# Kernel tuning notes

Hardware: AMD Instinct MI355X
Metric: run time of the kernel (lower is better)

Reference implementation:

```python
import jax, jax.numpy as jnp
import numpy as np

ALPHA = 0.025
BETA = 0.00025
V_TH = 1.0
EXP_TAU = 50.0          # tau_v / dt
T_NOW = 10.0            # current simulation step counter self.t
REFRAC_STEPS = 2        # refractory_period / dt
INV_TAU_V = float(np.exp(-1.0 / 50.0))   # exp(-dt/tau_v)
INV_TAU_I = float(np.exp(-1.0))          # exp(-dt/tau_i)
INV_TAU_V_PAIR = INV_TAU_V               # tau_v_pair defaults to tau_v
INV_TAU_I_PAIR = INV_TAU_I               # tau_i_pair defaults to tau_i

B, N = 32, 4096


def setup_inputs() -> dict:
    key = jax.random.key(0)
    ks = jax.random.split(key, 8)
    return {
        "inp": jax.random.normal(ks[0], (B, N), jnp.float32),
        "W_rec": jax.random.uniform(ks[1], (N, N), jnp.float32),  # nonneg dense adjacency weights
        "mem_pot": jax.random.normal(ks[2], (B, N), jnp.float32),
        "mem_cur": jax.random.normal(ks[3], (B, N), jnp.float32),
        "mem_pot_paired": jax.random.normal(ks[4], (B, N), jnp.float32),
        "mem_cur_paired": jax.random.normal(ks[5], (B, N), jnp.float32),
        "st": jnp.zeros((N,), jnp.float32),
        "refrac_neurons": jax.random.randint(ks[6], (B, N), 0, 3, jnp.int32),
    }


def reference(inp, W_rec, mem_pot, mem_cur, mem_pot_paired, mem_cur_paired, st, refrac_neurons):
    sign_mask = W_rec > 0  # torch: sign(W_rec) > 0 (weights are nonneg)

    # decrement refractory counters
    refrac = jnp.where(refrac_neurons > 0, refrac_neurons - 1, refrac_neurons)

    # threshold (ceil+clamp -> {0,1} spikes)
    S = jnp.clip(jnp.ceil(mem_pot - V_TH), 0.0, 1.0)                     # (B,N)
    S_paired = jnp.clip(jnp.ceil(mem_pot_paired - V_TH - ALPHA), 0.0, 1.0)

    # ---- plasticity weight update ----
    sp_max = S_paired.max(axis=0)            # (N,)
    st_new = jnp.where(S > 0, T_NOW, st)     # broadcasts (N,) -> (B,N), as in torch
    max_st = st_new.max(axis=0)              # (N,)
    # meshgrid(a,b) with ij indexing: |a-b|[i,j] = |max_st[i]-max_st[j]|
    diff = jnp.abs(max_st[:, None] - max_st[None, :])                    # (N,N)
    update_mask = (sp_max[:, None] > 0) & sign_mask                      # (N,N)
    updated = W_rec + BETA - jnp.where(update_mask,
                                       ALPHA * jnp.exp(diff / EXP_TAU),
                                       0.0)
    updated = jnp.clip(updated, 0.0, 1.0)
    W_new = jnp.where(sign_mask, updated, W_rec)

    # ---- integrate ----
    active = refrac == 0
    mem_cur_n = jnp.where(active, inp + S @ W_new + mem_cur, mem_cur)
    mem_cur_p_n = jnp.where(active, S @ W_new.T + mem_cur_paired, mem_cur_paired)
    mem_pot_n = jnp.where(active, mem_cur_n + mem_pot, mem_pot)
    mem_pot_p_n = jnp.where(active, mem_cur_p_n + mem_pot_paired, mem_pot_paired)

    # leak
    mem_pot_n = mem_pot_n * INV_TAU_V
    mem_cur_n = mem_cur_n * INV_TAU_I
    mem_pot_p_n = mem_pot_p_n * INV_TAU_V_PAIR
    mem_cur_p_n = mem_cur_p_n * INV_TAU_I_PAIR

    # reset spiked neurons
    mem_pot_n = jnp.where(S > 0, 0.0, mem_pot_n)
    mem_pot_p_n = jnp.where(S_paired > 0, 0.0, mem_pot_p_n)
    refrac_new = jnp.where(S > 0, REFRAC_STEPS, refrac)

    return S, mem_pot_n, W_new, mem_cur_n, mem_pot_p_n, mem_cur_p_n, refrac_new
```

## Files before the change

kernel.cpp:

```cpp
#include <hip/hip_runtime.h>
#include <cstdint>
#include <cstddef>

constexpr int N = 4096;
constexpr int B = 32;
constexpr int BN = B * N;
constexpr size_t NN = (size_t)N * N;
constexpr int KCHUNKS = 8;
constexpr int KC = N / KCHUNKS;

constexpr float ALPHA = 0.025f;
constexpr float BETA = 0.00025f;
constexpr float T_NOW = 10.0f;
constexpr float INV_EXP_TAU = 0.02f;
constexpr float INV_TAU_V = 0.98019867f;
constexpr float INV_TAU_I = 0.36787944f;

typedef __attribute__((ext_vector_type(8))) short short8;
typedef __attribute__((ext_vector_type(4))) float f32x4;

__device__ inline unsigned short f2bf(float f) {
  uint32_t u = __float_as_uint(f);
  u += 0x7FFFu + ((u >> 16) & 1u);
  return (unsigned short)(u >> 16);
}

__device__ inline float wupd(float w, float mrow, float frow, float mcol) {
  float d = fabsf(mrow - mcol);
  float u = w + BETA - frow * __expf(d * INV_EXP_TAU);
  u = fminf(fmaxf(u, 0.0f), 1.0f);
  return (w > 0.0f) ? u : w;
}

__global__ __launch_bounds__(256) void pass_a(
    const float* __restrict__ mem_pot, const float* __restrict__ mem_pot_p,
    const float* __restrict__ st, float* __restrict__ S_out,
    unsigned short* __restrict__ S_bf,
    uint32_t* __restrict__ maskS, uint32_t* __restrict__ maskSP,
    float* __restrict__ max_st, float* __restrict__ rowfac,
    float4* __restrict__ zero_region ) {
  int j = blockIdx.x * blockDim.x + threadIdx.x;
  if (j >= N) return;

  float4 z = {0.0f, 0.0f, 0.0f, 0.0f};
  #pragma unroll
  for (int k = 0; k < 16; ++k) zero_region[j + k * 4096] = z;

  float stj = st[j];
  uint32_t ms = 0u, msp = 0u;
  float maxv = -3.0e38f;
  #pragma unroll
  for (int b = 0; b < B; ++b) {
    float p = mem_pot[b * N + j];
    float pp = mem_pot_p[b * N + j];
    bool s = (p - 1.0f) > 0.0f;
    bool sp = ((pp - 1.0f) - ALPHA) > 0.0f;
    S_out[b * N + j] = s ? 1.0f : 0.0f;
    S_bf[b * N + j] = s ? 0x3F80u : 0u;
    ms |= (uint32_t)s << b;
    msp |= (uint32_t)sp << b;
    maxv = fmaxf(maxv, s ? T_NOW : stj);
  }
  maskS[j] = ms;
  maskSP[j] = msp;
  max_st[j] = maxv;
  rowfac[j] = msp ? ALPHA : 0.0f;
}

__global__ __launch_bounds__(256) void pass_fused(
    const float* __restrict__ W, const unsigned short* __restrict__ S_bf,
    const float* __restrict__ max_st, const float* __restrict__ rowfac,
    float* __restrict__ Wout, float* __restrict__ SW, float* __restrict__ SWT) {
  __shared__ float mstK[KC];
  __shared__ float facK[KC];

  int tid = threadIdx.x;
  int wv = tid >> 6;
  int lane = tid & 63;
  int ntile = blockIdx.x * 4 + wv;
  int j0 = ntile * 16;
  int kbase = blockIdx.y * KC;
  int gemm = blockIdx.z;
  int quad = lane >> 4;
  int nl = lane & 15;

  for (int t = tid; t < KC; t += 256) {
    mstK[t] = max_st[kbase + t];
    facK[t] = rowfac[kbase + t];
  }
  __syncthreads();

  f32x4 acc0 = {0.f, 0.f, 0.f, 0.f};
  f32x4 acc1 = {0.f, 0.f, 0.f, 0.f};
  const unsigned short* A0p = S_bf + (size_t)nl * N;
  const unsigned short* A1p = S_bf + (size_t)(nl + 16) * N;

  if (gemm == 0) {
    float mj = max_st[j0 + nl];
    #pragma unroll 2
    for (int it = 0; it < KC / 32; ++it) {
      int ko = it * 32 + quad * 8;
      int kg = kbase + ko;
      short8 a0 = *(const short8*)(A0p + kg);
      short8 a1 = *(const short8*)(A1p + kg);
      const float* wp = W + (size_t)kg * N + j0 + nl;
      float4 m4a = *(const float4*)(mstK + ko);
      float4 m4b = *(const float4*)(mstK + ko + 4);
      float4 f4a = *(const float4*)(facK + ko);
      float4 f4b = *(const float4*)(facK + ko + 4);
      float w[8];
      #pragma unroll
      for (int i = 0; i < 8; ++i) w[i] = wp[(size_t)i * N];
      short8 bf;
      bf[0] = (short)f2bf(wupd(w[0], m4a.x, f4a.x, mj));
      bf[1] = (short)f2bf(wupd(w[1], m4a.y, f4a.y, mj));
      bf[2] = (short)f2bf(wupd(w[2], m4a.z, f4a.z, mj));
      bf[3] = (short)f2bf(wupd(w[3], m4a.w, f4a.w, mj));
      bf[4] = (short)f2bf(wupd(w[4], m4b.x, f4b.x, mj));
      bf[5] = (short)f2bf(wupd(w[5], m4b.y, f4b.y, mj));
      bf[6] = (short)f2bf(wupd(w[6], m4b.z, f4b.z, mj));
      bf[7] = (short)f2bf(wupd(w[7], m4b.w, f4b.w, mj));
      acc0 = __builtin_amdgcn_mfma_f32_16x16x32_bf16(a0, bf, acc0, 0, 0, 0);
      acc1 = __builtin_amdgcn_mfma_f32_16x16x32_bf16(a1, bf, acc1, 0, 0, 0);
    }
  } else {
    float mi = max_st[j0 + nl];
    float fi = rowfac[j0 + nl];
    const float* __restrict__ Wr = W + (size_t)(j0 + nl) * N;
    float* __restrict__ Wor = Wout + (size_t)(j0 + nl) * N;
    #pragma unroll 2
    for (int it = 0; it < KC / 32; ++it) {
      int ko = it * 32 + quad * 8;
      int kg = kbase + ko;
      short8 a0 = *(const short8*)(A0p + kg);
      short8 a1 = *(const short8*)(A1p + kg);
      float4 f0 = *(const float4*)(Wr + kg);
      float4 f1 = *(const float4*)(Wr + kg + 4);
      float4 m4a = *(const float4*)(mstK + ko);
      float4 m4b = *(const float4*)(mstK + ko + 4);
      float4 u0, u1;
      u0.x = wupd(f0.x, mi, fi, m4a.x);
      u0.y = wupd(f0.y, mi, fi, m4a.y);
      u0.z = wupd(f0.z, mi, fi, m4a.z);
      u0.w = wupd(f0.w, mi, fi, m4a.w);
      u1.x = wupd(f1.x, mi, fi, m4b.x);
      u1.y = wupd(f1.y, mi, fi, m4b.y);
      u1.z = wupd(f1.z, mi, fi, m4b.z);
      u1.w = wupd(f1.w, mi, fi, m4b.w);
      *(float4*)(Wor + kg) = u0;
      *(float4*)(Wor + kg + 4) = u1;
      short8 bf;
      bf[0] = (short)f2bf(u0.x); bf[1] = (short)f2bf(u0.y);
      bf[2] = (short)f2bf(u0.z); bf[3] = (short)f2bf(u0.w);
      bf[4] = (short)f2bf(u1.x); bf[5] = (short)f2bf(u1.y);
      bf[6] = (short)f2bf(u1.z); bf[7] = (short)f2bf(u1.w);
      acc0 = __builtin_amdgcn_mfma_f32_16x16x32_bf16(a0, bf, acc0, 0, 0, 0);
      acc1 = __builtin_amdgcn_mfma_f32_16x16x32_bf16(a1, bf, acc1, 0, 0, 0);
    }
  }

  float* dst = (gemm == 0) ? SW : SWT;
  #pragma unroll
  for (int r = 0; r < 4; ++r) {
    atomicAdd(dst + (size_t)(quad * 4 + r) * N + j0 + nl, acc0[r]);
    atomicAdd(dst + (size_t)(16 + quad * 4 + r) * N + j0 + nl, acc1[r]);
  }
}

__global__ __launch_bounds__(256) void pass_d(
    const float* __restrict__ inp, const float* __restrict__ mem_pot,
    const float* __restrict__ mem_cur, const float* __restrict__ mem_pot_p,
    const float* __restrict__ mem_cur_p, const int* __restrict__ refrac_in,
    const uint32_t* __restrict__ maskS, const uint32_t* __restrict__ maskSP,
    const float* __restrict__ SWbuf, const float* __restrict__ SWTbuf,
    float* __restrict__ pot_out, float* __restrict__ cur_out,
    float* __restrict__ potp_out, float* __restrict__ curp_out,
    float* __restrict__ refrac_out) {
  int e = blockIdx.x * 256 + threadIdx.x;
  int b = e >> 12;
  int j = e & (N - 1);

  float SW = SWbuf[e];
  float SWT = SWTbuf[e];

  int r = refrac_in[e];
  int rd = (r > 0) ? (r - 1) : r;
  bool active = (rd == 0);
  bool s = (maskS[j] >> b) & 1u;
  bool sp = (maskSP[j] >> b) & 1u;
  float cur = mem_cur[e], pot = mem_pot[e];
  float curp = mem_cur_p[e], potp = mem_pot_p[e];

  float cur_n = active ? (inp[e] + SW + cur) : cur;
  float curp_n = active ? (SWT + curp) : curp;
  float pot_n = active ? (cur_n + pot) : pot;
  float potp_n = active ? (curp_n + potp) : potp;

  pot_n *= INV_TAU_V;
  cur_n *= INV_TAU_I;
  potp_n *= INV_TAU_V;
  curp_n *= INV_TAU_I;

  if (s) pot_n = 0.0f;
  if (sp) potp_n = 0.0f;
  int rn = s ? 2 : rd;

  pot_out[e] = pot_n;
  cur_out[e] = cur_n;
  potp_out[e] = potp_n;
  curp_out[e] = curp_n;
  refrac_out[e] = (float)rn;
}

extern "C" void kernel_launch(void* const* d_in, const int* in_sizes, int n_in,
                              void* d_out, int out_size, void* d_ws, size_t ws_size,
                              hipStream_t stream) {
  const float* inp = (const float*)d_in[0];
  const float* W = (const float*)d_in[1];
  const float* mem_pot = (const float*)d_in[2];
  const float* mem_cur = (const float*)d_in[3];
  const float* mem_pot_p = (const float*)d_in[4];
  const float* mem_cur_p = (const float*)d_in[5];
  const float* st = (const float*)d_in[6];
  const int* refrac = (const int*)d_in[7];

  float* out = (float*)d_out;
  float* S_out = out;
  float* pot_out = out + BN;
  float* W_out = out + 2 * (size_t)BN;
  float* cur_out = W_out + NN;
  float* potp_out = cur_out + BN;
  float* curp_out = potp_out + BN;
  float* refrac_out = curp_out + BN;

  uint32_t* maskS = (uint32_t*)d_ws;
  uint32_t* maskSP = maskS + N;
  float* max_st = (float*)(maskSP + N);
  float* rowfac = max_st + N;
  unsigned short* S_bf = (unsigned short*)(rowfac + N);
  float* SW = (float*)(S_bf + BN);
  float* SWT = SW + BN;

  pass_a<<<N / 256, 256, 0, stream>>>(mem_pot, mem_pot_p, st, S_out, S_bf,
                                      maskS, maskSP, max_st, rowfac,
                                      (float4*)SW);
  pass_fused<<<dim3(64, KCHUNKS, 2), 256, 0, stream>>>(W, S_bf, max_st, rowfac,
                                                       W_out, SW, SWT);
  pass_d<<<BN / 256, 256, 0, stream>>>(inp, mem_pot, mem_cur, mem_pot_p,
                                       mem_cur_p, refrac, maskS, maskSP,
                                       SW, SWT, pot_out, cur_out,
                                       potp_out, curp_out, refrac_out);
}
```

Before: 171.2 us.

## Replace atomic split-K accumulation with per-chunk partials and in-block LDS reduction

Each block now covers one 16-column tile, and its four waves split that block's K chunk among themselves. The per-wave MFMA accumulators are summed through shared memory, and each block writes a plain partial sum per K chunk. The final pass adds the four partials instead of relying on atomicAdd into zeroed buffers, so the zeroing in pass_a goes away. The W loads are software-prefetched one iteration ahead, and launch bounds request higher occupancy. In exchange the workspace traffic for partials grows, and the reduction adds a block-wide barrier.

New measurement: 175.8 us. +2.6%, slower.

```diff
diff --git a/kernel.cpp b/kernel.cpp
--- a/kernel.cpp
+++ b/kernel.cpp
@@ -6,8 +6,10 @@
 constexpr int B = 32;
 constexpr int BN = B * N;
 constexpr size_t NN = (size_t)N * N;
-constexpr int KCHUNKS = 8;
-constexpr int KC = N / KCHUNKS;
+constexpr int KCHUNKS = 4;
+constexpr int CHUNK = N / KCHUNKS;
+constexpr int KW = CHUNK / 4;
+constexpr int NIT = KW / 32;
 
 constexpr float ALPHA = 0.025f;
 constexpr float BETA = 0.00025f;
@@ -37,15 +39,9 @@
     const float* __restrict__ st, float* __restrict__ S_out,
     unsigned short* __restrict__ S_bf,
     uint32_t* __restrict__ maskS, uint32_t* __restrict__ maskSP,
-    float* __restrict__ max_st, float* __restrict__ rowfac,
-    float4* __restrict__ zero_region ) {
+    float* __restrict__ max_st, float* __restrict__ rowfac) {
   int j = blockIdx.x * blockDim.x + threadIdx.x;
   if (j >= N) return;
-
-  float4 z = {0.0f, 0.0f, 0.0f, 0.0f};
-  #pragma unroll
-  for (int k = 0; k < 16; ++k) zero_region[j + k * 4096] = z;
-
   float stj = st[j];
   uint32_t ms = 0u, msp = 0u;
   float maxv = -3.0e38f;
@@ -67,24 +63,25 @@
   rowfac[j] = msp ? ALPHA : 0.0f;
 }
 
-__global__ __launch_bounds__(256) void pass_fused(
+__global__ __launch_bounds__(256, 6) void pass_fused(
     const float* __restrict__ W, const unsigned short* __restrict__ S_bf,
     const float* __restrict__ max_st, const float* __restrict__ rowfac,
-    float* __restrict__ Wout, float* __restrict__ SW, float* __restrict__ SWT) {
-  __shared__ float mstK[KC];
-  __shared__ float facK[KC];
+    float* __restrict__ Wout, float* __restrict__ partSW,
+    float* __restrict__ partSWT) {
+  __shared__ float mstK[CHUNK];
+  __shared__ float facK[CHUNK];
+  __shared__ float red[4][32][17];
 
   int tid = threadIdx.x;
   int wv = tid >> 6;
   int lane = tid & 63;
-  int ntile = blockIdx.x * 4 + wv;
-  int j0 = ntile * 16;
-  int kbase = blockIdx.y * KC;
+  int j0 = blockIdx.x * 16;
+  int kbase = blockIdx.y * CHUNK;
   int gemm = blockIdx.z;
   int quad = lane >> 4;
   int nl = lane & 15;
 
-  for (int t = tid; t < KC; t += 256) {
+  for (int t = tid; t < CHUNK; t += 256) {
     mstK[t] = max_st[kbase + t];
     facK[t] = rowfac[kbase + t];
   }
@@ -94,23 +91,30 @@
   f32x4 acc1 = {0.f, 0.f, 0.f, 0.f};
   const unsigned short* A0p = S_bf + (size_t)nl * N;
   const unsigned short* A1p = S_bf + (size_t)(nl + 16) * N;
+  int kw = kbase + wv * KW;
 
   if (gemm == 0) {
     float mj = max_st[j0 + nl];
-    #pragma unroll 2
-    for (int it = 0; it < KC / 32; ++it) {
-      int ko = it * 32 + quad * 8;
-      int kg = kbase + ko;
+    const float* wp0 = W + (size_t)(kw + quad * 8) * N + j0 + nl;
+    float w[8];
+    #pragma unroll
+    for (int i = 0; i < 8; ++i) w[i] = wp0[(size_t)i * N];
+    #pragma unroll
+    for (int it = 0; it < NIT; ++it) {
+      int kloc = wv * KW + it * 32 + quad * 8;
+      int kg = kw + it * 32 + quad * 8;
       short8 a0 = *(const short8*)(A0p + kg);
       short8 a1 = *(const short8*)(A1p + kg);
-      const float* wp = W + (size_t)kg * N + j0 + nl;
-      float4 m4a = *(const float4*)(mstK + ko);
-      float4 m4b = *(const float4*)(mstK + ko + 4);
-      float4 f4a = *(const float4*)(facK + ko);
-      float4 f4b = *(const float4*)(facK + ko + 4);
-      float w[8];
-      #pragma unroll
-      for (int i = 0; i < 8; ++i) w[i] = wp[(size_t)i * N];
+      float wn[8];
+      if (it + 1 < NIT) {
+        const float* wpn = wp0 + (size_t)(it + 1) * 32 * N;
+        #pragma unroll
+        for (int i = 0; i < 8; ++i) wn[i] = wpn[(size_t)i * N];
+      }
+      float4 m4a = *(const float4*)(mstK + kloc);
+      float4 m4b = *(const float4*)(mstK + kloc + 4);
+      float4 f4a = *(const float4*)(facK + kloc);
+      float4 f4b = *(const float4*)(facK + kloc + 4);
       short8 bf;
       bf[0] = (short)f2bf(wupd(w[0], m4a.x, f4a.x, mj));
       bf[1] = (short)f2bf(wupd(w[1], m4a.y, f4a.y, mj));
@@ -122,22 +126,31 @@
       bf[7] = (short)f2bf(wupd(w[7], m4b.w, f4b.w, mj));
       acc0 = __builtin_amdgcn_mfma_f32_16x16x32_bf16(a0, bf, acc0, 0, 0, 0);
       acc1 = __builtin_amdgcn_mfma_f32_16x16x32_bf16(a1, bf, acc1, 0, 0, 0);
+      if (it + 1 < NIT) {
+        #pragma unroll
+        for (int i = 0; i < 8; ++i) w[i] = wn[i];
+      }
     }
   } else {
     float mi = max_st[j0 + nl];
     float fi = rowfac[j0 + nl];
-    const float* __restrict__ Wr = W + (size_t)(j0 + nl) * N;
-    float* __restrict__ Wor = Wout + (size_t)(j0 + nl) * N;
-    #pragma unroll 2
-    for (int it = 0; it < KC / 32; ++it) {
-      int ko = it * 32 + quad * 8;
-      int kg = kbase + ko;
+    const float* __restrict__ wrp = W + (size_t)(j0 + nl) * N + kw + quad * 8;
+    float* __restrict__ worp = Wout + (size_t)(j0 + nl) * N + kw + quad * 8;
+    float4 f0 = *(const float4*)(wrp);
+    float4 f1 = *(const float4*)(wrp + 4);
+    #pragma unroll
+    for (int it = 0; it < NIT; ++it) {
+      int kloc = wv * KW + it * 32 + quad * 8;
+      int kg = kw + it * 32 + quad * 8;
       short8 a0 = *(const short8*)(A0p + kg);
       short8 a1 = *(const short8*)(A1p + kg);
-      float4 f0 = *(const float4*)(Wr + kg);
-      float4 f1 = *(const float4*)(Wr + kg + 4);
-      float4 m4a = *(const float4*)(mstK + ko);
-      float4 m4b = *(const float4*)(mstK + ko + 4);
+      float4 g0, g1;
+      if (it + 1 < NIT) {
+        g0 = *(const float4*)(wrp + (it + 1) * 32);
+        g1 = *(const float4*)(wrp + (it + 1) * 32 + 4);
+      }
+      float4 m4a = *(const float4*)(mstK + kloc);
+      float4 m4b = *(const float4*)(mstK + kloc + 4);
       float4 u0, u1;
       u0.x = wupd(f0.x, mi, fi, m4a.x);
       u0.y = wupd(f0.y, mi, fi, m4a.y);
@@ -147,8 +160,8 @@
       u1.y = wupd(f1.y, mi, fi, m4b.y);
       u1.z = wupd(f1.z, mi, fi, m4b.z);
       u1.w = wupd(f1.w, mi, fi, m4b.w);
-      *(float4*)(Wor + kg) = u0;
-      *(float4*)(Wor + kg + 4) = u1;
+      *(float4*)(worp + it * 32) = u0;
+      *(float4*)(worp + it * 32 + 4) = u1;
       short8 bf;
       bf[0] = (short)f2bf(u0.x); bf[1] = (short)f2bf(u0.y);
       bf[2] = (short)f2bf(u0.z); bf[3] = (short)f2bf(u0.w);
@@ -156,14 +169,27 @@
       bf[6] = (short)f2bf(u1.z); bf[7] = (short)f2bf(u1.w);
       acc0 = __builtin_amdgcn_mfma_f32_16x16x32_bf16(a0, bf, acc0, 0, 0, 0);
       acc1 = __builtin_amdgcn_mfma_f32_16x16x32_bf16(a1, bf, acc1, 0, 0, 0);
+      if (it + 1 < NIT) { f0 = g0; f1 = g1; }
     }
   }
 
-  float* dst = (gemm == 0) ? SW : SWT;
   #pragma unroll
   for (int r = 0; r < 4; ++r) {
-    atomicAdd(dst + (size_t)(quad * 4 + r) * N + j0 + nl, acc0[r]);
-    atomicAdd(dst + (size_t)(16 + quad * 4 + r) * N + j0 + nl, acc1[r]);
+    red[wv][quad * 4 + r][nl] = acc0[r];
+    red[wv][16 + quad * 4 + r][nl] = acc1[r];
+  }
+  __syncthreads();
+  {
+    int row = tid >> 4;
+    int col = tid & 15;
+    float* part = (gemm == 0) ? partSW : partSWT;
+    size_t base = (size_t)blockIdx.y * BN + j0 + col;
+    float s0 = red[0][row][col] + red[1][row][col] +
+               red[2][row][col] + red[3][row][col];
+    float s1 = red[0][row + 16][col] + red[1][row + 16][col] +
+               red[2][row + 16][col] + red[3][row + 16][col];
+    part[base + (size_t)row * N] = s0;
+    part[base + (size_t)(row + 16) * N] = s1;
   }
 }
 
@@ -172,7 +198,7 @@
     const float* __restrict__ mem_cur, const float* __restrict__ mem_pot_p,
     const float* __restrict__ mem_cur_p, const int* __restrict__ refrac_in,
     const uint32_t* __restrict__ maskS, const uint32_t* __restrict__ maskSP,
-    const float* __restrict__ SWbuf, const float* __restrict__ SWTbuf,
+    const float* __restrict__ partSW, const float* __restrict__ partSWT,
     float* __restrict__ pot_out, float* __restrict__ cur_out,
     float* __restrict__ potp_out, float* __restrict__ curp_out,
     float* __restrict__ refrac_out) {
@@ -180,8 +206,12 @@
   int b = e >> 12;
   int j = e & (N - 1);
 
-  float SW = SWbuf[e];
-  float SWT = SWTbuf[e];
+  float SW = 0.0f, SWT = 0.0f;
+  #pragma unroll
+  for (int c = 0; c < KCHUNKS; ++c) {
+    SW += partSW[(size_t)c * BN + e];
+    SWT += partSWT[(size_t)c * BN + e];
+  }
 
   int r = refrac_in[e];
   int rd = (r > 0) ? (r - 1) : r;
@@ -238,16 +268,15 @@
   float* max_st = (float*)(maskSP + N);
   float* rowfac = max_st + N;
   unsigned short* S_bf = (unsigned short*)(rowfac + N);
-  float* SW = (float*)(S_bf + BN);
-  float* SWT = SW + BN;
+  float* partSW = (float*)(S_bf + BN);
+  float* partSWT = partSW + (size_t)KCHUNKS * BN;
 
   pass_a<<<N / 256, 256, 0, stream>>>(mem_pot, mem_pot_p, st, S_out, S_bf,
-                                      maskS, maskSP, max_st, rowfac,
-                                      (float4*)SW);
-  pass_fused<<<dim3(64, KCHUNKS, 2), 256, 0, stream>>>(W, S_bf, max_st, rowfac,
-                                                       W_out, SW, SWT);
+                                      maskS, maskSP, max_st, rowfac);
+  pass_fused<<<dim3(N / 16, KCHUNKS, 2), 256, 0, stream>>>(
+      W, S_bf, max_st, rowfac, W_out, partSW, partSWT);
   pass_d<<<BN / 256, 256, 0, stream>>>(inp, mem_pot, mem_cur, mem_pot_p,
                                        mem_cur_p, refrac, maskS, maskSP,
-                                       SW, SWT, pot_out, cur_out,
+                                       partSW, partSWT, pot_out, cur_out,
                                        potp_out, curp_out, refrac_out);
 }
```
